# Kernel tuning notes

Measured on AMD Instinct MI355X. Metric: run time of the kernel, lower is better.

The kernel has to match this reference:

```python
import jax, jax.numpy as jnp
import numpy as np

WS = 8            # window_size
N = WS * WS       # tokens per window = 64
DIM = 512
H = 16            # num_heads
HD = DIM // H     # head_dim = 32
P = 16            # linformer proj_dim
B = 2048          # number of windows (batch * windows per image)


def _relative_position_index(ws: int) -> np.ndarray:
    coords = np.stack(np.meshgrid(np.arange(ws), np.arange(ws), indexing='ij'))  # [2,ws,ws]
    cf = coords.reshape(2, -1)                                                   # [2, N]
    rel = cf[:, :, None] - cf[:, None, :]                                        # [2, N, N]
    rel = rel.transpose(1, 2, 0).astype(np.int64)                                # [N, N, 2]
    rel[:, :, 0] += ws - 1
    rel[:, :, 1] += ws - 1
    rel[:, :, 0] *= 2 * ws - 1
    return rel.sum(-1)  # [N, N]

REL_INDEX = jnp.asarray(_relative_position_index(WS))  # int, [N, N]


def setup_inputs() -> dict:
    key = jax.random.key(0)
    ks = jax.random.split(key, 9)
    s = 0.02
    return {
        'x': jax.random.normal(ks[0], (B, N, DIM), dtype=jnp.float32),
        'w_qkv': jax.random.normal(ks[1], (DIM, 3 * DIM), dtype=jnp.float32) * s,
        'b_qkv': jax.random.normal(ks[2], (3 * DIM,), dtype=jnp.float32) * s,
        'w_proj': jax.random.normal(ks[3], (DIM, DIM), dtype=jnp.float32) * s,
        'b_proj': jax.random.normal(ks[4], (DIM,), dtype=jnp.float32) * s,
        'w_k': jax.random.normal(ks[5], (P, N), dtype=jnp.float32) * s,   # Linear(N -> P), torch weight layout [out,in]
        'w_v': jax.random.normal(ks[6], (P, N), dtype=jnp.float32) * s,
        'bias_table': jax.random.normal(ks[7], ((2 * WS - 1) ** 2, H), dtype=jnp.float32) * s,
    }


def reference(x, w_qkv, b_qkv, w_proj, b_proj, w_k, w_v, bias_table):
    B_, n, c = x.shape
    scale = HD ** -0.5
    qkv = (x @ w_qkv + b_qkv).reshape(B_, n, 3, H, HD)
    qkv = jnp.transpose(qkv, (2, 0, 3, 1, 4))          # [3, B, H, N, hd]
    q, k, v = qkv[0] * scale, qkv[1], qkv[2]           # each [B, H, N, hd]
    # Linformer projection along token axis N -> P
    k = jnp.einsum('bhnd,pn->bhpd', k, w_k)            # [B, H, P, hd]
    v = jnp.einsum('bhnd,pn->bhpd', v, w_v)            # [B, H, P, hd]
    attn = jnp.einsum('bhnd,bhpd->bhnp', q, k)         # [B, H, N, P]
    # relative position bias gather, sliced to projected length P
    bias = bias_table[REL_INDEX.reshape(-1)].reshape(n, n, H)  # [N, N, H]
    bias = jnp.transpose(bias, (2, 0, 1))[None, :, :, :attn.shape[-1]]  # [1, H, N, P]
    attn = jax.nn.softmax(attn + bias, axis=-1)
    out = jnp.einsum('bhnp,bhpd->bhnd', attn, v)       # [B, H, N, hd]
    out = jnp.transpose(out, (0, 2, 1, 3)).reshape(B_, n, c)
    return out @ w_proj + b_proj
```

## Files before the change

### kernel.cpp

```cpp
#include <hip/hip_runtime.h>

typedef __bf16 bf16;
typedef __attribute__((ext_vector_type(8))) __bf16 bf16x8;
typedef __attribute__((ext_vector_type(4))) __bf16 bf16x4;
typedef __attribute__((ext_vector_type(4))) float f32x4;
typedef __attribute__((ext_vector_type(4))) short s16x4;

#define SCALE 0.17677669529663687f

#define PHASE_FENCE() asm volatile("" ::: "memory")

__device__ __forceinline__ f32x4 mfma16(bf16x8 a, bf16x8 b, f32x4 c) {
  return __builtin_amdgcn_mfma_f32_16x16x32_bf16(a, b, c, 0, 0, 0);
}

__device__ __forceinline__ f32x4 mfma16k16(bf16x4 a, bf16x4 b, f32x4 c) {
#if __has_builtin(__builtin_amdgcn_mfma_f32_16x16x16bf16_1k)
  return __builtin_amdgcn_mfma_f32_16x16x16bf16_1k(
      __builtin_bit_cast(s16x4, a), __builtin_bit_cast(s16x4, b), c, 0, 0, 0);
#else
  asm("v_mfma_f32_16x16x16_bf16 %0, %1, %2, %0" : "+v"(c) : "v"(a), "v"(b));
  return c;
#endif
}

__global__ void prep_weights(const float* __restrict__ w_qkv,
                             const float* __restrict__ w_proj,
                             bf16* __restrict__ wt, bf16* __restrict__ wpt) {
  __shared__ float tile[32][33];
  int b = blockIdx.x;
  const float* src; bf16* dst; int C, tk, tc;
  if (b < 768) {
    src = w_qkv; dst = wt; C = 1536; tk = (b & 15) * 32; tc = (b >> 4) * 32;
  } else {
    b -= 768; src = w_proj; dst = wpt; C = 512; tk = (b & 15) * 32; tc = (b >> 4) * 32;
  }
  int tx = threadIdx.x & 31, ty = threadIdx.x >> 5;
#pragma unroll
  for (int i = 0; i < 4; i++)
    tile[ty + i * 8][tx] = src[(size_t)(tk + ty + i * 8) * C + tc + tx];
  __syncthreads();
#pragma unroll
  for (int i = 0; i < 4; i++)
    dst[(size_t)(tc + ty + i * 8) * 512 + tk + tx] = (bf16)tile[tx][ty + i * 8];
}

__launch_bounds__(512, 4)
__global__ void ewattn(const float* __restrict__ x,
                       const float* __restrict__ b_qkv,
                       const float* __restrict__ w_k,
                       const float* __restrict__ w_v,
                       const float* __restrict__ bias_table,
                       const float* __restrict__ b_proj,
                       const bf16* __restrict__ wt,
                       const bf16* __restrict__ wpt,
                       float* __restrict__ out) {
  __shared__ bf16 xs[64][520];

  const int tid  = threadIdx.x;
  const int lane = tid & 63;
  const int wid  = tid >> 6;
  const int l15  = lane & 15;
  const int quad = lane >> 4;
  const int win  = blockIdx.x;
  const float* xw = x + (size_t)win * (64 * 512);

#pragma unroll
  for (int j = 0; j < 8; j++) {
    int i = tid + j * 512;
    int r = i >> 6, c8 = (i & 63) * 8;
    float4 v0 = *reinterpret_cast<const float4*>(xw + r * 512 + c8);
    float4 v1 = *reinterpret_cast<const float4*>(xw + r * 512 + c8 + 4);
    bf16x8 p;
    p[0] = (bf16)v0.x; p[1] = (bf16)v0.y; p[2] = (bf16)v0.z; p[3] = (bf16)v0.w;
    p[4] = (bf16)v1.x; p[5] = (bf16)v1.y; p[6] = (bf16)v1.z; p[7] = (bf16)v1.w;
    *reinterpret_cast<bf16x8*>(&xs[r][c8]) = p;
  }
  __syncthreads();

  bf16x4 vpf[2][2];
  bf16x4 ap[2][4];

#pragma unroll
  for (int hi = 0; hi < 2; hi++) {
    const int h = wid * 2 + hi;

    bf16x4 kb[4][2];
    {
      f32x4 kacc[4][2];
#pragma unroll
      for (int tt = 0; tt < 4; tt++)
#pragma unroll
        for (int nt = 0; nt < 2; nt++) kacc[tt][nt] = f32x4{0.f,0.f,0.f,0.f};
      for (int kt = 0; kt < 16; kt++) {
        bf16x8 af[4];
#pragma unroll
        for (int tt = 0; tt < 4; tt++)
          af[tt] = *(const bf16x8*)&xs[tt * 16 + l15][kt * 32 + quad * 8];
        bf16x8 bwk[2];
#pragma unroll
        for (int nt = 0; nt < 2; nt++)
          bwk[nt] = *(const bf16x8*)&wt[(size_t)(512 + h * 32 + nt * 16 + l15) * 512 + kt * 32 + quad * 8];
#pragma unroll
        for (int tt = 0; tt < 4; tt++)
#pragma unroll
          for (int nt = 0; nt < 2; nt++)
            kacc[tt][nt] = mfma16(af[tt], bwk[nt], kacc[tt][nt]);
      }
#pragma unroll
      for (int nt = 0; nt < 2; nt++) {
        float bk = b_qkv[512 + h * 32 + nt * 16 + l15];
#pragma unroll
        for (int tt = 0; tt < 4; tt++)
#pragma unroll
          for (int r = 0; r < 4; r++)
            kb[tt][nt][r] = (bf16)(kacc[tt][nt][r] + bk);
      }
    }
    PHASE_FENCE();

    bf16x4 vb[4][2];
    {
      f32x4 vacc[4][2];
#pragma unroll
      for (int tt = 0; tt < 4; tt++)
#pragma unroll
        for (int nt = 0; nt < 2; nt++) vacc[tt][nt] = f32x4{0.f,0.f,0.f,0.f};
      for (int kt = 0; kt < 16; kt++) {
        bf16x8 af[4];
#pragma unroll
        for (int tt = 0; tt < 4; tt++)
          af[tt] = *(const bf16x8*)&xs[tt * 16 + l15][kt * 32 + quad * 8];
        bf16x8 bwv[2];
#pragma unroll
        for (int nt = 0; nt < 2; nt++)
          bwv[nt] = *(const bf16x8*)&wt[(size_t)(1024 + h * 32 + nt * 16 + l15) * 512 + kt * 32 + quad * 8];
#pragma unroll
        for (int tt = 0; tt < 4; tt++)
#pragma unroll
          for (int nt = 0; nt < 2; nt++)
            vacc[tt][nt] = mfma16(af[tt], bwv[nt], vacc[tt][nt]);
      }
#pragma unroll
      for (int nt = 0; nt < 2; nt++) {
        float bv = b_qkv[1024 + h * 32 + nt * 16 + l15];
#pragma unroll
        for (int tt = 0; tt < 4; tt++)
#pragma unroll
          for (int r = 0; r < 4; r++)
            vb[tt][nt][r] = (bf16)(vacc[tt][nt][r] + bv);
      }
    }
    PHASE_FENCE();

    bf16x4 kpf[2];
    {
      bf16x4 wkf[4], wvf[4];
#pragma unroll
      for (int tt = 0; tt < 4; tt++) {
        float4 a = *(const float4*)&w_k[l15 * 64 + tt * 16 + quad * 4];
        float4 b = *(const float4*)&w_v[l15 * 64 + tt * 16 + quad * 4];
        wkf[tt][0] = (bf16)a.x; wkf[tt][1] = (bf16)a.y; wkf[tt][2] = (bf16)a.z; wkf[tt][3] = (bf16)a.w;
        wvf[tt][0] = (bf16)b.x; wvf[tt][1] = (bf16)b.y; wvf[tt][2] = (bf16)b.z; wvf[tt][3] = (bf16)b.w;
      }
      f32x4 kpacc[2], vpacc[2];
      kpacc[0] = kpacc[1] = vpacc[0] = vpacc[1] = f32x4{0.f,0.f,0.f,0.f};
#pragma unroll
      for (int tt = 0; tt < 4; tt++)
#pragma unroll
        for (int nt = 0; nt < 2; nt++) {
          kpacc[nt] = mfma16k16(kb[tt][nt], wkf[tt], kpacc[nt]);
          vpacc[nt] = mfma16k16(wvf[tt], vb[tt][nt], vpacc[nt]);
        }
#pragma unroll
      for (int nt = 0; nt < 2; nt++)
#pragma unroll
        for (int r = 0; r < 4; r++) {
          kpf[nt][r]     = (bf16)kpacc[nt][r];
          vpf[hi][nt][r] = (bf16)vpacc[nt][r];
        }
    }
    PHASE_FENCE();

    bf16x4 qb[2][4];
    {
      f32x4 qacc[2][4];
#pragma unroll
      for (int ct = 0; ct < 2; ct++)
#pragma unroll
        for (int tt = 0; tt < 4; tt++) qacc[ct][tt] = f32x4{0.f,0.f,0.f,0.f};
      for (int kt = 0; kt < 16; kt++) {
        bf16x8 aw[2];
#pragma unroll
        for (int ct = 0; ct < 2; ct++)
          aw[ct] = *(const bf16x8*)&wt[(size_t)(h * 32 + ct * 16 + l15) * 512 + kt * 32 + quad * 8];
        bf16x8 bx[4];
#pragma unroll
        for (int tt = 0; tt < 4; tt++)
          bx[tt] = *(const bf16x8*)&xs[tt * 16 + l15][kt * 32 + quad * 8];
#pragma unroll
        for (int ct = 0; ct < 2; ct++)
#pragma unroll
          for (int tt = 0; tt < 4; tt++)
            qacc[ct][tt] = mfma16(aw[ct], bx[tt], qacc[ct][tt]);
      }
#pragma unroll
      for (int ct = 0; ct < 2; ct++)
#pragma unroll
        for (int tt = 0; tt < 4; tt++)
#pragma unroll
          for (int r = 0; r < 4; r++)
            qb[ct][tt][r] = (bf16)((qacc[ct][tt][r] +
                                    b_qkv[h * 32 + ct * 16 + quad * 4 + r]) * SCALE);
    }
    PHASE_FENCE();

#pragma unroll
    for (int tt = 0; tt < 4; tt++) {
      f32x4 att = mfma16k16(kpf[0], qb[0][tt], f32x4{0.f,0.f,0.f,0.f});
      att = mfma16k16(kpf[1], qb[1][tt], att);
      int n = tt * 16 + l15;
      float e[4], s = 0.f;
#pragma unroll
      for (int r = 0; r < 4; r++) {
        int p = quad * 4 + r;
        int rel = ((n >> 3) - (p >> 3) + 7) * 15 + ((n & 7) - (p & 7) + 7);
        e[r] = __expf(att[r] + bias_table[rel * 16 + h]);
        s += e[r];
      }
      s += __shfl_xor(s, 16); s += __shfl_xor(s, 32);
      float rc = __builtin_amdgcn_rcpf(s);
#pragma unroll
      for (int r = 0; r < 4; r++) ap[hi][tt][r] = (bf16)(e[r] * rc);
    }
    PHASE_FENCE();
  }
  __syncthreads();

#pragma unroll
  for (int hi = 0; hi < 2; hi++) {
    const int h = wid * 2 + hi;
#pragma unroll
    for (int tt = 0; tt < 4; tt++)
#pragma unroll
      for (int nd = 0; nd < 2; nd++) {
        f32x4 ov = mfma16k16(ap[hi][tt], vpf[hi][nd], f32x4{0.f,0.f,0.f,0.f});
#pragma unroll
        for (int r = 0; r < 4; r++)
          xs[tt * 16 + quad * 4 + r][h * 32 + nd * 16 + l15] = (bf16)ov[r];
      }
  }
  __syncthreads();

  {
    f32x4 oacc[4][4];
#pragma unroll
    for (int mt = 0; mt < 4; mt++)
#pragma unroll
      for (int nt = 0; nt < 4; nt++) oacc[mt][nt] = f32x4{0.f,0.f,0.f,0.f};
    for (int kt = 0; kt < 16; kt++) {
      bf16x8 af[4];
#pragma unroll
      for (int mt = 0; mt < 4; mt++)
        af[mt] = *(const bf16x8*)&xs[mt * 16 + l15][kt * 32 + quad * 8];
      bf16x8 bw[4];
#pragma unroll
      for (int nt = 0; nt < 4; nt++)
        bw[nt] = *(const bf16x8*)&wpt[(size_t)(wid * 64 + nt * 16 + l15) * 512 + kt * 32 + quad * 8];
#pragma unroll
      for (int mt = 0; mt < 4; mt++)
#pragma unroll
        for (int nt = 0; nt < 4; nt++)
          oacc[mt][nt] = mfma16(af[mt], bw[nt], oacc[mt][nt]);
    }
    float* ow = out + (size_t)win * (64 * 512);
#pragma unroll
    for (int nt = 0; nt < 4; nt++) {
      int c = wid * 64 + nt * 16 + l15;
      float bp = b_proj[c];
#pragma unroll
      for (int mt = 0; mt < 4; mt++)
#pragma unroll
        for (int r = 0; r < 4; r++)
          ow[(size_t)(mt * 16 + quad * 4 + r) * 512 + c] = oacc[mt][nt][r] + bp;
    }
  }
}

extern "C" void kernel_launch(void* const* d_in, const int* in_sizes, int n_in,
                              void* d_out, int out_size, void* d_ws, size_t ws_size,
                              hipStream_t stream) {
  const float* x          = (const float*)d_in[0];
  const float* w_qkv      = (const float*)d_in[1];
  const float* b_qkv      = (const float*)d_in[2];
  const float* w_proj     = (const float*)d_in[3];
  const float* b_proj     = (const float*)d_in[4];
  const float* w_k        = (const float*)d_in[5];
  const float* w_v        = (const float*)d_in[6];
  const float* bias_table = (const float*)d_in[7];
  (void)in_sizes; (void)n_in; (void)out_size; (void)ws_size;

  bf16* wt  = (bf16*)d_ws;
  bf16* wpt = wt + 1536 * 512;

  prep_weights<<<1024, 256, 0, stream>>>(w_qkv, w_proj, wt, wpt);
  ewattn<<<2048, 512, 0, stream>>>(x, b_qkv, w_k, w_v, bias_table, b_proj,
                                   wt, wpt, (float*)d_out);
}
```

Measured before the change: 970.2 us.

## Split attention across two blocks per window and move output projection to separate kernel

The fused kernel is split into two launches. The attention kernel now uses two blocks per window with one head per wave, so each block does half the per-window QKV work and there are twice as many blocks. The attention output is staged as bf16 in the second half of each window's slice of the output buffer. A second kernel reads it back and runs the output projection, writing fp32 over the same window slice. This removes the serial two-heads-per-wave loop at the cost of converting x twice per window, an extra global round trip for the attention output, and a kernel launch. The LDS row stride is also padded from 520 to 536.

```diff
diff --git a/kernel.cpp b/kernel.cpp
--- a/kernel.cpp
+++ b/kernel.cpp
@@ -9,6 +9,8 @@
 #define SCALE 0.17677669529663687f
 
 #define PHASE_FENCE() asm volatile("" ::: "memory")
+
+#define XS_LD 536
 
 __device__ __forceinline__ f32x4 mfma16(bf16x8 a, bf16x8 b, f32x4 c) {
   return __builtin_amdgcn_mfma_f32_16x16x32_bf16(a, b, c, 0, 0, 0);
@@ -46,23 +48,22 @@
 }
 
 __launch_bounds__(512, 4)
-__global__ void ewattn(const float* __restrict__ x,
-                       const float* __restrict__ b_qkv,
-                       const float* __restrict__ w_k,
-                       const float* __restrict__ w_v,
-                       const float* __restrict__ bias_table,
-                       const float* __restrict__ b_proj,
-                       const bf16* __restrict__ wt,
-                       const bf16* __restrict__ wpt,
-                       float* __restrict__ out) {
-  __shared__ bf16 xs[64][520];
+__global__ void ewattn_a(const float* __restrict__ x,
+                         const float* __restrict__ b_qkv,
+                         const float* __restrict__ w_k,
+                         const float* __restrict__ w_v,
+                         const float* __restrict__ bias_table,
+                         const bf16* __restrict__ wt,
+                         float* out) {
+  __shared__ bf16 xs[64][XS_LD];
 
   const int tid  = threadIdx.x;
   const int lane = tid & 63;
   const int wid  = tid >> 6;
   const int l15  = lane & 15;
   const int quad = lane >> 4;
-  const int win  = blockIdx.x;
+  const int win  = blockIdx.x >> 1;
+  const int h    = (blockIdx.x & 1) * 8 + wid;
   const float* xw = x + (size_t)win * (64 * 512);
 
 #pragma unroll
@@ -78,212 +79,222 @@
   }
   __syncthreads();
 
-  bf16x4 vpf[2][2];
-  bf16x4 ap[2][4];
-
-#pragma unroll
-  for (int hi = 0; hi < 2; hi++) {
-    const int h = wid * 2 + hi;
-
-    bf16x4 kb[4][2];
-    {
-      f32x4 kacc[4][2];
-#pragma unroll
-      for (int tt = 0; tt < 4; tt++)
-#pragma unroll
-        for (int nt = 0; nt < 2; nt++) kacc[tt][nt] = f32x4{0.f,0.f,0.f,0.f};
-      for (int kt = 0; kt < 16; kt++) {
-        bf16x8 af[4];
-#pragma unroll
-        for (int tt = 0; tt < 4; tt++)
-          af[tt] = *(const bf16x8*)&xs[tt * 16 + l15][kt * 32 + quad * 8];
-        bf16x8 bwk[2];
-#pragma unroll
-        for (int nt = 0; nt < 2; nt++)
-          bwk[nt] = *(const bf16x8*)&wt[(size_t)(512 + h * 32 + nt * 16 + l15) * 512 + kt * 32 + quad * 8];
-#pragma unroll
-        for (int tt = 0; tt < 4; tt++)
-#pragma unroll
-          for (int nt = 0; nt < 2; nt++)
-            kacc[tt][nt] = mfma16(af[tt], bwk[nt], kacc[tt][nt]);
-      }
-#pragma unroll
-      for (int nt = 0; nt < 2; nt++) {
-        float bk = b_qkv[512 + h * 32 + nt * 16 + l15];
-#pragma unroll
-        for (int tt = 0; tt < 4; tt++)
-#pragma unroll
-          for (int r = 0; r < 4; r++)
-            kb[tt][nt][r] = (bf16)(kacc[tt][nt][r] + bk);
-      }
-    }
-    PHASE_FENCE();
-
-    bf16x4 vb[4][2];
-    {
-      f32x4 vacc[4][2];
-#pragma unroll
-      for (int tt = 0; tt < 4; tt++)
-#pragma unroll
-        for (int nt = 0; nt < 2; nt++) vacc[tt][nt] = f32x4{0.f,0.f,0.f,0.f};
-      for (int kt = 0; kt < 16; kt++) {
-        bf16x8 af[4];
-#pragma unroll
-        for (int tt = 0; tt < 4; tt++)
-          af[tt] = *(const bf16x8*)&xs[tt * 16 + l15][kt * 32 + quad * 8];
-        bf16x8 bwv[2];
-#pragma unroll
-        for (int nt = 0; nt < 2; nt++)
-          bwv[nt] = *(const bf16x8*)&wt[(size_t)(1024 + h * 32 + nt * 16 + l15) * 512 + kt * 32 + quad * 8];
-#pragma unroll
-        for (int tt = 0; tt < 4; tt++)
-#pragma unroll
-          for (int nt = 0; nt < 2; nt++)
-            vacc[tt][nt] = mfma16(af[tt], bwv[nt], vacc[tt][nt]);
-      }
-#pragma unroll
-      for (int nt = 0; nt < 2; nt++) {
-        float bv = b_qkv[1024 + h * 32 + nt * 16 + l15];
-#pragma unroll
-        for (int tt = 0; tt < 4; tt++)
-#pragma unroll
-          for (int r = 0; r < 4; r++)
-            vb[tt][nt][r] = (bf16)(vacc[tt][nt][r] + bv);
-      }
-    }
-    PHASE_FENCE();
-
-    bf16x4 kpf[2];
-    {
-      bf16x4 wkf[4], wvf[4];
-#pragma unroll
-      for (int tt = 0; tt < 4; tt++) {
-        float4 a = *(const float4*)&w_k[l15 * 64 + tt * 16 + quad * 4];
-        float4 b = *(const float4*)&w_v[l15 * 64 + tt * 16 + quad * 4];
-        wkf[tt][0] = (bf16)a.x; wkf[tt][1] = (bf16)a.y; wkf[tt][2] = (bf16)a.z; wkf[tt][3] = (bf16)a.w;
-        wvf[tt][0] = (bf16)b.x; wvf[tt][1] = (bf16)b.y; wvf[tt][2] = (bf16)b.z; wvf[tt][3] = (bf16)b.w;
-      }
-      f32x4 kpacc[2], vpacc[2];
-      kpacc[0] = kpacc[1] = vpacc[0] = vpacc[1] = f32x4{0.f,0.f,0.f,0.f};
-#pragma unroll
-      for (int tt = 0; tt < 4; tt++)
-#pragma unroll
-        for (int nt = 0; nt < 2; nt++) {
-          kpacc[nt] = mfma16k16(kb[tt][nt], wkf[tt], kpacc[nt]);
-          vpacc[nt] = mfma16k16(wvf[tt], vb[tt][nt], vpacc[nt]);
-        }
-#pragma unroll
-      for (int nt = 0; nt < 2; nt++)
-#pragma unroll
-        for (int r = 0; r < 4; r++) {
-          kpf[nt][r]     = (bf16)kpacc[nt][r];
-          vpf[hi][nt][r] = (bf16)vpacc[nt][r];
-        }
-    }
-    PHASE_FENCE();
-
-    bf16x4 qb[2][4];
-    {
-      f32x4 qacc[2][4];
-#pragma unroll
-      for (int ct = 0; ct < 2; ct++)
-#pragma unroll
-        for (int tt = 0; tt < 4; tt++) qacc[ct][tt] = f32x4{0.f,0.f,0.f,0.f};
-      for (int kt = 0; kt < 16; kt++) {
-        bf16x8 aw[2];
-#pragma unroll
-        for (int ct = 0; ct < 2; ct++)
-          aw[ct] = *(const bf16x8*)&wt[(size_t)(h * 32 + ct * 16 + l15) * 512 + kt * 32 + quad * 8];
-        bf16x8 bx[4];
-#pragma unroll
-        for (int tt = 0; tt < 4; tt++)
-          bx[tt] = *(const bf16x8*)&xs[tt * 16 + l15][kt * 32 + quad * 8];
-#pragma unroll
-        for (int ct = 0; ct < 2; ct++)
-#pragma unroll
-          for (int tt = 0; tt < 4; tt++)
-            qacc[ct][tt] = mfma16(aw[ct], bx[tt], qacc[ct][tt]);
-      }
-#pragma unroll
-      for (int ct = 0; ct < 2; ct++)
-#pragma unroll
-        for (int tt = 0; tt < 4; tt++)
-#pragma unroll
-          for (int r = 0; r < 4; r++)
-            qb[ct][tt][r] = (bf16)((qacc[ct][tt][r] +
-                                    b_qkv[h * 32 + ct * 16 + quad * 4 + r]) * SCALE);
-    }
-    PHASE_FENCE();
-
-#pragma unroll
-    for (int tt = 0; tt < 4; tt++) {
-      f32x4 att = mfma16k16(kpf[0], qb[0][tt], f32x4{0.f,0.f,0.f,0.f});
-      att = mfma16k16(kpf[1], qb[1][tt], att);
-      int n = tt * 16 + l15;
-      float e[4], s = 0.f;
-#pragma unroll
-      for (int r = 0; r < 4; r++) {
-        int p = quad * 4 + r;
-        int rel = ((n >> 3) - (p >> 3) + 7) * 15 + ((n & 7) - (p & 7) + 7);
-        e[r] = __expf(att[r] + bias_table[rel * 16 + h]);
-        s += e[r];
-      }
-      s += __shfl_xor(s, 16); s += __shfl_xor(s, 32);
-      float rc = __builtin_amdgcn_rcpf(s);
-#pragma unroll
-      for (int r = 0; r < 4; r++) ap[hi][tt][r] = (bf16)(e[r] * rc);
-    }
-    PHASE_FENCE();
-  }
-  __syncthreads();
-
-#pragma unroll
-  for (int hi = 0; hi < 2; hi++) {
-    const int h = wid * 2 + hi;
+  bf16x4 kb[4][2];
+  {
+    f32x4 kacc[4][2];
 #pragma unroll
     for (int tt = 0; tt < 4; tt++)
 #pragma unroll
-      for (int nd = 0; nd < 2; nd++) {
-        f32x4 ov = mfma16k16(ap[hi][tt], vpf[hi][nd], f32x4{0.f,0.f,0.f,0.f});
-#pragma unroll
-        for (int r = 0; r < 4; r++)
-          xs[tt * 16 + quad * 4 + r][h * 32 + nd * 16 + l15] = (bf16)ov[r];
-      }
-  }
-  __syncthreads();
-
-  {
-    f32x4 oacc[4][4];
-#pragma unroll
-    for (int mt = 0; mt < 4; mt++)
-#pragma unroll
-      for (int nt = 0; nt < 4; nt++) oacc[mt][nt] = f32x4{0.f,0.f,0.f,0.f};
+      for (int nt = 0; nt < 2; nt++) kacc[tt][nt] = f32x4{0.f,0.f,0.f,0.f};
     for (int kt = 0; kt < 16; kt++) {
       bf16x8 af[4];
 #pragma unroll
-      for (int mt = 0; mt < 4; mt++)
-        af[mt] = *(const bf16x8*)&xs[mt * 16 + l15][kt * 32 + quad * 8];
-      bf16x8 bw[4];
+      for (int tt = 0; tt < 4; tt++)
+        af[tt] = *(const bf16x8*)&xs[tt * 16 + l15][kt * 32 + quad * 8];
+      bf16x8 bwk[2];
+#pragma unroll
+      for (int nt = 0; nt < 2; nt++)
+        bwk[nt] = *(const bf16x8*)&wt[(size_t)(512 + h * 32 + nt * 16 + l15) * 512 + kt * 32 + quad * 8];
+#pragma unroll
+      for (int tt = 0; tt < 4; tt++)
+#pragma unroll
+        for (int nt = 0; nt < 2; nt++)
+          kacc[tt][nt] = mfma16(af[tt], bwk[nt], kacc[tt][nt]);
+    }
+#pragma unroll
+    for (int nt = 0; nt < 2; nt++) {
+      float bk = b_qkv[512 + h * 32 + nt * 16 + l15];
+#pragma unroll
+      for (int tt = 0; tt < 4; tt++)
+#pragma unroll
+        for (int r = 0; r < 4; r++)
+          kb[tt][nt][r] = (bf16)(kacc[tt][nt][r] + bk);
+    }
+  }
+  PHASE_FENCE();
+
+  bf16x4 vb[4][2];
+  {
+    f32x4 vacc[4][2];
+#pragma unroll
+    for (int tt = 0; tt < 4; tt++)
+#pragma unroll
+      for (int nt = 0; nt < 2; nt++) vacc[tt][nt] = f32x4{0.f,0.f,0.f,0.f};
+    for (int kt = 0; kt < 16; kt++) {
+      bf16x8 af[4];
+#pragma unroll
+      for (int tt = 0; tt < 4; tt++)
+        af[tt] = *(const bf16x8*)&xs[tt * 16 + l15][kt * 32 + quad * 8];
+      bf16x8 bwv[2];
+#pragma unroll
+      for (int nt = 0; nt < 2; nt++)
+        bwv[nt] = *(const bf16x8*)&wt[(size_t)(1024 + h * 32 + nt * 16 + l15) * 512 + kt * 32 + quad * 8];
+#pragma unroll
+      for (int tt = 0; tt < 4; tt++)
+#pragma unroll
+        for (int nt = 0; nt < 2; nt++)
+          vacc[tt][nt] = mfma16(af[tt], bwv[nt], vacc[tt][nt]);
+    }
+#pragma unroll
+    for (int nt = 0; nt < 2; nt++) {
+      float bv = b_qkv[1024 + h * 32 + nt * 16 + l15];
+#pragma unroll
+      for (int tt = 0; tt < 4; tt++)
+#pragma unroll
+        for (int r = 0; r < 4; r++)
+          vb[tt][nt][r] = (bf16)(vacc[tt][nt][r] + bv);
+    }
+  }
+  PHASE_FENCE();
+
+  bf16x4 kpf[2], vpf[2];
+  {
+    bf16x4 wkf[4], wvf[4];
+#pragma unroll
+    for (int tt = 0; tt < 4; tt++) {
+      float4 a = *(const float4*)&w_k[l15 * 64 + tt * 16 + quad * 4];
+      float4 b = *(const float4*)&w_v[l15 * 64 + tt * 16 + quad * 4];
+      wkf[tt][0] = (bf16)a.x; wkf[tt][1] = (bf16)a.y; wkf[tt][2] = (bf16)a.z; wkf[tt][3] = (bf16)a.w;
+      wvf[tt][0] = (bf16)b.x; wvf[tt][1] = (bf16)b.y; wvf[tt][2] = (bf16)b.z; wvf[tt][3] = (bf16)b.w;
+    }
+    f32x4 kpacc[2], vpacc[2];
+    kpacc[0] = kpacc[1] = vpacc[0] = vpacc[1] = f32x4{0.f,0.f,0.f,0.f};
+#pragma unroll
+    for (int tt = 0; tt < 4; tt++)
+#pragma unroll
+      for (int nt = 0; nt < 2; nt++) {
+        kpacc[nt] = mfma16k16(kb[tt][nt], wkf[tt], kpacc[nt]);
+        vpacc[nt] = mfma16k16(wvf[tt], vb[tt][nt], vpacc[nt]);
+      }
+#pragma unroll
+    for (int nt = 0; nt < 2; nt++)
+#pragma unroll
+      for (int r = 0; r < 4; r++) {
+        kpf[nt][r] = (bf16)kpacc[nt][r];
+        vpf[nt][r] = (bf16)vpacc[nt][r];
+      }
+  }
+  PHASE_FENCE();
+
+  bf16x4 qb[2][4];
+  {
+    f32x4 qacc[2][4];
+#pragma unroll
+    for (int ct = 0; ct < 2; ct++)
+#pragma unroll
+      for (int tt = 0; tt < 4; tt++) qacc[ct][tt] = f32x4{0.f,0.f,0.f,0.f};
+    for (int kt = 0; kt < 16; kt++) {
+      bf16x8 aw[2];
+#pragma unroll
+      for (int ct = 0; ct < 2; ct++)
+        aw[ct] = *(const bf16x8*)&wt[(size_t)(h * 32 + ct * 16 + l15) * 512 + kt * 32 + quad * 8];
+      bf16x8 bx[4];
+#pragma unroll
+      for (int tt = 0; tt < 4; tt++)
+        bx[tt] = *(const bf16x8*)&xs[tt * 16 + l15][kt * 32 + quad * 8];
+#pragma unroll
+      for (int ct = 0; ct < 2; ct++)
+#pragma unroll
+        for (int tt = 0; tt < 4; tt++)
+          qacc[ct][tt] = mfma16(aw[ct], bx[tt], qacc[ct][tt]);
+    }
+#pragma unroll
+    for (int ct = 0; ct < 2; ct++)
+#pragma unroll
+      for (int tt = 0; tt < 4; tt++)
+#pragma unroll
+        for (int r = 0; r < 4; r++)
+          qb[ct][tt][r] = (bf16)((qacc[ct][tt][r] +
+                                  b_qkv[h * 32 + ct * 16 + quad * 4 + r]) * SCALE);
+  }
+  PHASE_FENCE();
+
+  bf16* aoW = reinterpret_cast<bf16*>(reinterpret_cast<char*>(out) +
+                                      ((size_t)win * 131072 + 65536));
+#pragma unroll
+  for (int tt = 0; tt < 4; tt++) {
+    f32x4 att = mfma16k16(kpf[0], qb[0][tt], f32x4{0.f,0.f,0.f,0.f});
+    att = mfma16k16(kpf[1], qb[1][tt], att);
+    int n = tt * 16 + l15;
+    float e[4], s = 0.f;
+#pragma unroll
+    for (int r = 0; r < 4; r++) {
+      int p = quad * 4 + r;
+      int rel = ((n >> 3) - (p >> 3) + 7) * 15 + ((n & 7) - (p & 7) + 7);
+      e[r] = __expf(att[r] + bias_table[rel * 16 + h]);
+      s += e[r];
+    }
+    s += __shfl_xor(s, 16); s += __shfl_xor(s, 32);
+    float rc = __builtin_amdgcn_rcpf(s);
+    bf16x4 ap;
+#pragma unroll
+    for (int r = 0; r < 4; r++) ap[r] = (bf16)(e[r] * rc);
+#pragma unroll
+    for (int nd = 0; nd < 2; nd++) {
+      f32x4 ov = mfma16k16(ap, vpf[nd], f32x4{0.f,0.f,0.f,0.f});
+#pragma unroll
+      for (int r = 0; r < 4; r++) {
+        int token = tt * 16 + quad * 4 + r;
+        aoW[token * 512 + h * 32 + nd * 16 + l15] = (bf16)ov[r];
+      }
+    }
+  }
+}
+
+__launch_bounds__(512, 4)
+__global__ void oproj(const float* __restrict__ b_proj,
+                      const bf16* __restrict__ wpt,
+                      float* out) {
+  __shared__ bf16 as_[64][XS_LD];
+
+  const int tid  = threadIdx.x;
+  const int lane = tid & 63;
+  const int wid  = tid >> 6;
+  const int l15  = lane & 15;
+  const int quad = lane >> 4;
+  const int mb   = blockIdx.x;
+
+  const bf16* aoR = reinterpret_cast<const bf16*>(reinterpret_cast<const char*>(out) +
+                                                  ((size_t)mb * 131072 + 65536));
+#pragma unroll
+  for (int j = 0; j < 8; j++) {
+    int i = tid + j * 512;
+    int r = i >> 6, c8 = (i & 63) * 8;
+    *reinterpret_cast<bf16x8*>(&as_[r][c8]) =
+        *reinterpret_cast<const bf16x8*>(&aoR[r * 512 + c8]);
+  }
+  __syncthreads();
+
+  f32x4 oacc[4][4];
+#pragma unroll
+  for (int mt = 0; mt < 4; mt++)
+#pragma unroll
+    for (int nt = 0; nt < 4; nt++) oacc[mt][nt] = f32x4{0.f,0.f,0.f,0.f};
+  for (int kt = 0; kt < 16; kt++) {
+    bf16x8 af[4];
+#pragma unroll
+    for (int mt = 0; mt < 4; mt++)
+      af[mt] = *(const bf16x8*)&as_[mt * 16 + l15][kt * 32 + quad * 8];
+    bf16x8 bw[4];
+#pragma unroll
+    for (int nt = 0; nt < 4; nt++)
+      bw[nt] = *(const bf16x8*)&wpt[(size_t)(wid * 64 + nt * 16 + l15) * 512 + kt * 32 + quad * 8];
+#pragma unroll
+    for (int mt = 0; mt < 4; mt++)
 #pragma unroll
       for (int nt = 0; nt < 4; nt++)
-        bw[nt] = *(const bf16x8*)&wpt[(size_t)(wid * 64 + nt * 16 + l15) * 512 + kt * 32 + quad * 8];
-#pragma unroll
-      for (int mt = 0; mt < 4; mt++)
-#pragma unroll
-        for (int nt = 0; nt < 4; nt++)
-          oacc[mt][nt] = mfma16(af[mt], bw[nt], oacc[mt][nt]);
-    }
-    float* ow = out + (size_t)win * (64 * 512);
-#pragma unroll
-    for (int nt = 0; nt < 4; nt++) {
-      int c = wid * 64 + nt * 16 + l15;
-      float bp = b_proj[c];
-#pragma unroll
-      for (int mt = 0; mt < 4; mt++)
-#pragma unroll
-        for (int r = 0; r < 4; r++)
-          ow[(size_t)(mt * 16 + quad * 4 + r) * 512 + c] = oacc[mt][nt][r] + bp;
-    }
+        oacc[mt][nt] = mfma16(af[mt], bw[nt], oacc[mt][nt]);
+  }
+  float* ow = out + (size_t)mb * (64 * 512);
+#pragma unroll
+  for (int nt = 0; nt < 4; nt++) {
+    int c = wid * 64 + nt * 16 + l15;
+    float bp = b_proj[c];
+#pragma unroll
+    for (int mt = 0; mt < 4; mt++)
+#pragma unroll
+      for (int r = 0; r < 4; r++)
+        ow[(size_t)(mt * 16 + quad * 4 + r) * 512 + c] = oacc[mt][nt][r] + bp;
   }
 }
 
@@ -304,6 +315,7 @@
   bf16* wpt = wt + 1536 * 512;
 
   prep_weights<<<1024, 256, 0, stream>>>(w_qkv, w_proj, wt, wpt);
-  ewattn<<<2048, 512, 0, stream>>>(x, b_qkv, w_k, w_v, bias_table, b_proj,
-                                   wt, wpt, (float*)d_out);
-}
+  ewattn_a<<<4096, 512, 0, stream>>>(x, b_qkv, w_k, w_v, bias_table,
+                                     wt, (float*)d_out);
+  oproj<<<2048, 512, 0, stream>>>(b_proj, wpt, (float*)d_out);
+}
```

New measurement: 1.016 ms. 1.05x slower.
